# Kernel optimization log

Measured on AMD Instinct MI355X. Metric: run time of the kernel, lower is better.

Reference implementation:

```python
import jax, jax.numpy as jnp
import numpy as np
import math

B, C, H, W = 8, 64, 64, 64

def setup_inputs() -> dict:
    key = jax.random.key(0)
    k1, k2 = jax.random.split(key)
    x1 = jax.random.normal(k1, (B, C, H, W), dtype=jnp.float32)
    x2 = jax.random.normal(k2, (B, C, H, W), dtype=jnp.float32)
    return {"x1": x1, "x2": x2}

def reference(x1, x2):
    b, c, h, w = x1.shape
    # flatten spatial dims -> tokens: [B, HW, C]
    x1f = x1.reshape(b, c, h * w).transpose(0, 2, 1)
    x2f = x2.reshape(b, c, h * w).transpose(0, 2, 1)
    scale = 1.0 / math.sqrt(c)
    # direction A: queries from x1, keys/values from x2
    scores_a = jnp.einsum('bqc,bkc->bqk', x1f, x2f) * scale  # [B, HW, HW]
    out_a = jnp.einsum('bqk,bkc->bqc', jax.nn.softmax(scores_a, axis=-1), x2f)
    # direction B: queries from x2, keys/values from x1
    scores_b = jnp.einsum('bqc,bkc->bqk', x2f, x1f) * scale
    out_b = jnp.einsum('bqk,bkc->bqc', jax.nn.softmax(scores_b, axis=-1), x1f)
    out = (out_a + out_b).transpose(0, 2, 1).reshape(b, c, h, w)
    return out
```

## Files before the change

### kernel.cpp

```cpp
#include <hip/hip_runtime.h>
#include <hip/hip_bf16.h>
#include <stdint.h>


#define TT 4096
#define CC 64
#define NB 8

typedef float f32x4 __attribute__((ext_vector_type(4)));
typedef float f32x4a __attribute__((ext_vector_type(4), may_alias));
typedef short s16x8 __attribute__((ext_vector_type(8)));
typedef unsigned int u32x2a __attribute__((ext_vector_type(2), may_alias));
typedef unsigned int u32x4a __attribute__((ext_vector_type(4), may_alias));
typedef float f32a __attribute__((may_alias));

static __device__ __forceinline__ unsigned fbits(float x) { return __float_as_uint(x); }
static __device__ __forceinline__ ushort bf16of(float v) {
    return (ushort)((fbits(v) + 0x8000u) >> 16);
}
static __device__ __forceinline__ unsigned pack2(float a, float b) {
    return __builtin_amdgcn_perm(fbits(b) + 0x8000u, fbits(a) + 0x8000u, 0x07060302u);
}
static __device__ __forceinline__ s16x8 load_frag(const void* p) {
    u32x4a t = *(const u32x4a*)p;
    return __builtin_bit_cast(s16x8, t);
}

#define SQC1 0.4246609177f

__global__ void prep_k(const float* __restrict__ x1, const float* __restrict__ x2,
                       ushort* __restrict__ kt, ushort* __restrict__ vt) {
    const int inp = blockIdx.z, b = blockIdx.y, tt = blockIdx.x;
    const float* src = (inp == 0 ? x1 : x2) + (size_t)b * CC * TT;
    const size_t plane = (size_t)TT * CC;
    ushort* kd = kt + (size_t)(inp * NB + b) * plane;
    ushort* vd = vt + (size_t)(inp * NB + b) * plane;
    __shared__ ushort lds[64][72];
    const int tid = threadIdx.x;
    const int c  = tid >> 2;
    const int tg = tid & 3;
    const float* srow = src + (size_t)c * TT + tt * 64 + tg * 16;
    unsigned hw[8];
#pragma unroll
    for (int i = 0; i < 4; ++i) {
        f32x4a v = *(const f32x4a*)(srow + i * 4);
        hw[2 * i]     = pack2(v[0], v[1]);
        hw[2 * i + 1] = pack2(v[2], v[3]);
#pragma unroll
        for (int k = 0; k < 4; ++k) lds[tg * 16 + i * 4 + k][c] = bf16of(v[k] * SQC1);
    }
    {
        ushort* vchunk = vd + (((size_t)tt * 2 + (tg >> 1)) * 4 + (c >> 4)) * 512;
        const int l16v = c & 15;
        const int q0v  = (tg & 1) * 2;
        u32x4a w0 = {hw[0], hw[1], hw[2], hw[3]};
        u32x4a w1 = {hw[4], hw[5], hw[6], hw[7]};
        *(u32x4a*)(vchunk + (size_t)(q0v * 16 + l16v) * 8)       = w0;
        *(u32x4a*)(vchunk + (size_t)((q0v + 1) * 16 + l16v) * 8) = w1;
    }
    __syncthreads();
    const int mt   = tid >> 6;
    const int quad = (tid >> 4) & 3;
    const int l16  = tid & 15;
    const int t    = mt * 16 + l16;
#pragma unroll
    for (int ch = 0; ch < 2; ++ch) {
        u32x4a w = *(const u32x4a*)&lds[t][ch * 32 + quad * 8];
        *(u32x4a*)(kd + (((size_t)tt * 4 + mt) * 2 + ch) * 512 +
                   (size_t)(quad * 16 + l16) * 8) = w;
    }
}

__global__ __launch_bounds__(256, 3)
void attn_fused_k(const ushort* __restrict__ kt, const ushort* __restrict__ vt,
                  float* __restrict__ out) {
    const int b    = blockIdx.x & 7;
    const int pair = (blockIdx.x >> 3) & 1;
    const int qt   = blockIdx.x >> 4;
    const int tid  = threadIdx.x;
    const int wave = tid >> 6;
    const int lane = tid & 63;
    const int quad = lane >> 4;
    const int l16  = lane & 15;
    const int dir  = wave & 1;
    const int ks   = wave >> 1;
    const int q0   = qt * 64 + pair * 32;

    const size_t plane = (size_t)TT * CC;
    const ushort* Qp = kt + (size_t)((dir == 0 ? 0 : NB) + b) * plane + (size_t)lane * 8;
    const ushort* Kp = kt + (size_t)((dir == 0 ? NB : 0) + b) * plane + (size_t)lane * 8;
    const ushort* Vp = vt + (size_t)((dir == 0 ? NB : 0) + b) * plane + (size_t)lane * 8;

    __shared__ __align__(16) ushort pbuf[4][2][16][72];
    __shared__ float lpx[4][2][16];
    f32a* xbuf = (f32a*)&pbuf[0][0][0][0];

    s16x8 qf[2][2];
#pragma unroll
    for (int rb = 0; rb < 2; ++rb)
#pragma unroll
        for (int ch = 0; ch < 2; ++ch)
            qf[rb][ch] = load_frag(Qp + (((size_t)qt * 4 + pair * 2 + rb) * 2 + ch) * 512);

    f32x4 accO[2][4];
#pragma unroll
    for (int rb = 0; rb < 2; ++rb)
#pragma unroll
        for (int ct = 0; ct < 4; ++ct) accO[rb][ct] = (f32x4){0.f, 0.f, 0.f, 0.f};
    float lp[2] = {0.f, 0.f};

    s16x8 kA0, kA1, kA2, kA3, kA4, kA5, kA6, kA7;

    auto loadK = [&](int j) {
        const ushort* p = Kp + (size_t)(ks * 32 + j) * 4096;
        kA0 = load_frag(p);          kA1 = load_frag(p + 512);
        kA2 = load_frag(p + 1024);   kA3 = load_frag(p + 1536);
        kA4 = load_frag(p + 2048);   kA5 = load_frag(p + 2560);
        kA6 = load_frag(p + 3072);   kA7 = load_frag(p + 3584);
    };

    auto SmT = [&](s16x8 kc0, s16x8 kc1, int mt) {
#pragma unroll
        for (int rb = 0; rb < 2; ++rb) {
            f32x4 s = (f32x4){0.f, 0.f, 0.f, 0.f};
            s = __builtin_amdgcn_mfma_f32_16x16x32_bf16(kc0, qf[rb][0], s, 0, 0, 0);
            s = __builtin_amdgcn_mfma_f32_16x16x32_bf16(kc1, qf[rb][1], s, 0, 0, 0);
            float p0 = __builtin_amdgcn_exp2f(s[0]);
            float p1 = __builtin_amdgcn_exp2f(s[1]);
            float p2 = __builtin_amdgcn_exp2f(s[2]);
            float p3 = __builtin_amdgcn_exp2f(s[3]);
            lp[rb] += (p0 + p1) + (p2 + p3);
            u32x2a w;
            w[0] = pack2(p0, p1);
            w[1] = pack2(p2, p3);
            *(u32x2a*)&pbuf[wave][rb][l16][mt * 16 + quad * 4] = w;
        }
    };
    auto PVphase = [&](int j) {
        const ushort* p = Vp + (size_t)(ks * 32 + j) * 4096;
        s16x8 v0 = load_frag(p);           s16x8 v1 = load_frag(p + 512);
        s16x8 v2 = load_frag(p + 1024);    s16x8 v3 = load_frag(p + 1536);
        s16x8 v4 = load_frag(p + 2048);    s16x8 v5 = load_frag(p + 2560);
        s16x8 v6 = load_frag(p + 3072);    s16x8 v7 = load_frag(p + 3584);
        s16x8 pf0a = load_frag(&pbuf[wave][0][l16][quad * 8]);
        s16x8 pf1a = load_frag(&pbuf[wave][1][l16][quad * 8]);
        accO[0][0] = __builtin_amdgcn_mfma_f32_16x16x32_bf16(v0, pf0a, accO[0][0], 0, 0, 0);
        accO[1][0] = __builtin_amdgcn_mfma_f32_16x16x32_bf16(v0, pf1a, accO[1][0], 0, 0, 0);
        accO[0][1] = __builtin_amdgcn_mfma_f32_16x16x32_bf16(v1, pf0a, accO[0][1], 0, 0, 0);
        accO[1][1] = __builtin_amdgcn_mfma_f32_16x16x32_bf16(v1, pf1a, accO[1][1], 0, 0, 0);
        accO[0][2] = __builtin_amdgcn_mfma_f32_16x16x32_bf16(v2, pf0a, accO[0][2], 0, 0, 0);
        accO[1][2] = __builtin_amdgcn_mfma_f32_16x16x32_bf16(v2, pf1a, accO[1][2], 0, 0, 0);
        accO[0][3] = __builtin_amdgcn_mfma_f32_16x16x32_bf16(v3, pf0a, accO[0][3], 0, 0, 0);
        accO[1][3] = __builtin_amdgcn_mfma_f32_16x16x32_bf16(v3, pf1a, accO[1][3], 0, 0, 0);
        s16x8 pf0b = load_frag(&pbuf[wave][0][l16][32 + quad * 8]);
        s16x8 pf1b = load_frag(&pbuf[wave][1][l16][32 + quad * 8]);
        accO[0][0] = __builtin_amdgcn_mfma_f32_16x16x32_bf16(v4, pf0b, accO[0][0], 0, 0, 0);
        accO[1][0] = __builtin_amdgcn_mfma_f32_16x16x32_bf16(v4, pf1b, accO[1][0], 0, 0, 0);
        accO[0][1] = __builtin_amdgcn_mfma_f32_16x16x32_bf16(v5, pf0b, accO[0][1], 0, 0, 0);
        accO[1][1] = __builtin_amdgcn_mfma_f32_16x16x32_bf16(v5, pf1b, accO[1][1], 0, 0, 0);
        accO[0][2] = __builtin_amdgcn_mfma_f32_16x16x32_bf16(v6, pf0b, accO[0][2], 0, 0, 0);
        accO[1][2] = __builtin_amdgcn_mfma_f32_16x16x32_bf16(v6, pf1b, accO[1][2], 0, 0, 0);
        accO[0][3] = __builtin_amdgcn_mfma_f32_16x16x32_bf16(v7, pf0b, accO[0][3], 0, 0, 0);
        accO[1][3] = __builtin_amdgcn_mfma_f32_16x16x32_bf16(v7, pf1b, accO[1][3], 0, 0, 0);
    };

    loadK(0);
#pragma unroll 1
    for (int j = 0; j < 32; ++j) {
        __syncthreads();
        SmT(kA0, kA1, 0); SmT(kA2, kA3, 1); SmT(kA4, kA5, 2); SmT(kA6, kA7, 3);
        if (j < 31) loadK(j + 1);
        PVphase(j);
    }

    float inv[2];
#pragma unroll
    for (int rb = 0; rb < 2; ++rb) {
        float l = lp[rb];
        l += __shfl_xor(l, 16);
        l += __shfl_xor(l, 32);
        lp[rb] = l;
        if (lane < 16) lpx[wave][rb][l16] = l;
    }
    __syncthreads();
#pragma unroll
    for (int rb = 0; rb < 2; ++rb)
        inv[rb] = __builtin_amdgcn_rcpf(lp[rb] + lpx[wave ^ 2][rb][l16]);

    const int g = (ks << 1) | dir;
#pragma unroll 1
    for (int ph = 3; ph >= 1; --ph) {
        if (g == ph) {
#pragma unroll
            for (int rb = 0; rb < 2; ++rb)
#pragma unroll
                for (int ct = 0; ct < 4; ++ct)
#pragma unroll
                    for (int r = 0; r < 4; ++r) {
                        const int slot = (rb * 16 + ct * 4 + r) * 64 + lane;
                        float v = accO[rb][ct][r] * inv[rb];
                        if (ph == 3) xbuf[slot] = v;
                        else xbuf[slot] += v;
                    }
        }
        __syncthreads();
    }
    if (g == 0) {
        float* ob = out + (size_t)b * plane;
#pragma unroll
        for (int rb = 0; rb < 2; ++rb)
#pragma unroll
            for (int ct = 0; ct < 4; ++ct)
#pragma unroll
                for (int r = 0; r < 4; ++r) {
                    float v = accO[rb][ct][r] * inv[rb] +
                              xbuf[(rb * 16 + ct * 4 + r) * 64 + lane];
                    ob[(size_t)(ct * 16 + quad * 4 + r) * TT + q0 + rb * 16 + l16] = v;
                }
    }
}

extern "C" void kernel_launch(void* const* d_in, const int* in_sizes, int n_in,
                              void* d_out, int out_size, void* d_ws, size_t ws_size,
                              hipStream_t stream) {
    const float* x1 = (const float*)d_in[0];
    const float* x2 = (const float*)d_in[1];
    ushort* kt = (ushort*)d_ws;
    ushort* vt = (ushort*)d_ws + (size_t)2 * NB * TT * CC;

    hipLaunchKernelGGL(prep_k, dim3(TT / 64, NB, 2), dim3(256), 0, stream, x1, x2, kt, vt);
    hipLaunchKernelGGL(attn_fused_k, dim3(64 * NB * 2), dim3(256), 0, stream,
                       kt, vt, (float*)d_out);
}
```

Measured before the change: 180.1 us.

## Widen attention blocks to 8 waves with 64 queries and pipelined S/PV phases

```diff
diff --git a/kernel.cpp b/kernel.cpp
--- a/kernel.cpp
+++ b/kernel.cpp
@@ -71,57 +71,63 @@
     }
 }
 
-__global__ __launch_bounds__(256, 3)
+__global__ __attribute__((amdgpu_flat_work_group_size(512, 512)))
 void attn_fused_k(const ushort* __restrict__ kt, const ushort* __restrict__ vt,
                   float* __restrict__ out) {
     const int b    = blockIdx.x & 7;
-    const int pair = (blockIdx.x >> 3) & 1;
-    const int qt   = blockIdx.x >> 4;
+    const int qt   = blockIdx.x >> 3;
     const int tid  = threadIdx.x;
     const int wave = tid >> 6;
     const int lane = tid & 63;
     const int quad = lane >> 4;
     const int l16  = lane & 15;
     const int dir  = wave & 1;
-    const int ks   = wave >> 1;
-    const int q0   = qt * 64 + pair * 32;
+    const int ksq  = wave >> 1;
 
     const size_t plane = (size_t)TT * CC;
     const ushort* Qp = kt + (size_t)((dir == 0 ? 0 : NB) + b) * plane + (size_t)lane * 8;
     const ushort* Kp = kt + (size_t)((dir == 0 ? NB : 0) + b) * plane + (size_t)lane * 8;
     const ushort* Vp = vt + (size_t)((dir == 0 ? NB : 0) + b) * plane + (size_t)lane * 8;
 
-    __shared__ __align__(16) ushort pbuf[4][2][16][72];
-    __shared__ float lpx[4][2][16];
-    f32a* xbuf = (f32a*)&pbuf[0][0][0][0];
-
-    s16x8 qf[2][2];
-#pragma unroll
-    for (int rb = 0; rb < 2; ++rb)
+    __shared__ __align__(16) ushort pbuf[8][2][4][16][72];
+    __shared__ float lpx[8][4][16];
+    f32a* xbuf = (f32a*)&pbuf[0][0][0][0][0];
+
+    s16x8 qf[4][2];
+#pragma unroll
+    for (int rb = 0; rb < 4; ++rb)
 #pragma unroll
         for (int ch = 0; ch < 2; ++ch)
-            qf[rb][ch] = load_frag(Qp + (((size_t)qt * 4 + pair * 2 + rb) * 2 + ch) * 512);
-
-    f32x4 accO[2][4];
-#pragma unroll
-    for (int rb = 0; rb < 2; ++rb)
+            qf[rb][ch] = load_frag(Qp + (((size_t)qt * 4 + rb) * 2 + ch) * 512);
+
+    f32x4 accO[4][4];
+#pragma unroll
+    for (int rb = 0; rb < 4; ++rb)
 #pragma unroll
         for (int ct = 0; ct < 4; ++ct) accO[rb][ct] = (f32x4){0.f, 0.f, 0.f, 0.f};
-    float lp[2] = {0.f, 0.f};
-
-    s16x8 kA0, kA1, kA2, kA3, kA4, kA5, kA6, kA7;
+    float lp[4] = {0.f, 0.f, 0.f, 0.f};
+
+    s16x8 k0, k1, k2, k3, k4, k5, k6, k7;
+    s16x8 v0, v1, v2, v3, v4, v5, v6, v7;
 
     auto loadK = [&](int j) {
-        const ushort* p = Kp + (size_t)(ks * 32 + j) * 4096;
-        kA0 = load_frag(p);          kA1 = load_frag(p + 512);
-        kA2 = load_frag(p + 1024);   kA3 = load_frag(p + 1536);
-        kA4 = load_frag(p + 2048);   kA5 = load_frag(p + 2560);
-        kA6 = load_frag(p + 3072);   kA7 = load_frag(p + 3584);
-    };
-
-    auto SmT = [&](s16x8 kc0, s16x8 kc1, int mt) {
-#pragma unroll
-        for (int rb = 0; rb < 2; ++rb) {
+        const ushort* p = Kp + (size_t)(ksq * 16 + j) * 4096;
+        k0 = load_frag(p);          k1 = load_frag(p + 512);
+        k2 = load_frag(p + 1024);   k3 = load_frag(p + 1536);
+        k4 = load_frag(p + 2048);   k5 = load_frag(p + 2560);
+        k6 = load_frag(p + 3072);   k7 = load_frag(p + 3584);
+    };
+    auto loadV = [&](int j) {
+        const ushort* p = Vp + (size_t)(ksq * 16 + j) * 4096;
+        v0 = load_frag(p);          v1 = load_frag(p + 512);
+        v2 = load_frag(p + 1024);   v3 = load_frag(p + 1536);
+        v4 = load_frag(p + 2048);   v5 = load_frag(p + 2560);
+        v6 = load_frag(p + 3072);   v7 = load_frag(p + 3584);
+    };
+
+    auto SmT = [&](s16x8 kc0, s16x8 kc1, int mt, int par) {
+#pragma unroll
+        for (int rb = 0; rb < 4; ++rb) {
             f32x4 s = (f32x4){0.f, 0.f, 0.f, 0.f};
             s = __builtin_amdgcn_mfma_f32_16x16x32_bf16(kc0, qf[rb][0], s, 0, 0, 0);
             s = __builtin_amdgcn_mfma_f32_16x16x32_bf16(kc1, qf[rb][1], s, 0, 0, 0);
@@ -133,49 +139,54 @@
             u32x2a w;
             w[0] = pack2(p0, p1);
             w[1] = pack2(p2, p3);
-            *(u32x2a*)&pbuf[wave][rb][l16][mt * 16 + quad * 4] = w;
-        }
-    };
-    auto PVphase = [&](int j) {
-        const ushort* p = Vp + (size_t)(ks * 32 + j) * 4096;
-        s16x8 v0 = load_frag(p);           s16x8 v1 = load_frag(p + 512);
-        s16x8 v2 = load_frag(p + 1024);    s16x8 v3 = load_frag(p + 1536);
-        s16x8 v4 = load_frag(p + 2048);    s16x8 v5 = load_frag(p + 2560);
-        s16x8 v6 = load_frag(p + 3072);    s16x8 v7 = load_frag(p + 3584);
-        s16x8 pf0a = load_frag(&pbuf[wave][0][l16][quad * 8]);
-        s16x8 pf1a = load_frag(&pbuf[wave][1][l16][quad * 8]);
-        accO[0][0] = __builtin_amdgcn_mfma_f32_16x16x32_bf16(v0, pf0a, accO[0][0], 0, 0, 0);
-        accO[1][0] = __builtin_amdgcn_mfma_f32_16x16x32_bf16(v0, pf1a, accO[1][0], 0, 0, 0);
-        accO[0][1] = __builtin_amdgcn_mfma_f32_16x16x32_bf16(v1, pf0a, accO[0][1], 0, 0, 0);
-        accO[1][1] = __builtin_amdgcn_mfma_f32_16x16x32_bf16(v1, pf1a, accO[1][1], 0, 0, 0);
-        accO[0][2] = __builtin_amdgcn_mfma_f32_16x16x32_bf16(v2, pf0a, accO[0][2], 0, 0, 0);
-        accO[1][2] = __builtin_amdgcn_mfma_f32_16x16x32_bf16(v2, pf1a, accO[1][2], 0, 0, 0);
-        accO[0][3] = __builtin_amdgcn_mfma_f32_16x16x32_bf16(v3, pf0a, accO[0][3], 0, 0, 0);
-        accO[1][3] = __builtin_amdgcn_mfma_f32_16x16x32_bf16(v3, pf1a, accO[1][3], 0, 0, 0);
-        s16x8 pf0b = load_frag(&pbuf[wave][0][l16][32 + quad * 8]);
-        s16x8 pf1b = load_frag(&pbuf[wave][1][l16][32 + quad * 8]);
-        accO[0][0] = __builtin_amdgcn_mfma_f32_16x16x32_bf16(v4, pf0b, accO[0][0], 0, 0, 0);
-        accO[1][0] = __builtin_amdgcn_mfma_f32_16x16x32_bf16(v4, pf1b, accO[1][0], 0, 0, 0);
-        accO[0][1] = __builtin_amdgcn_mfma_f32_16x16x32_bf16(v5, pf0b, accO[0][1], 0, 0, 0);
-        accO[1][1] = __builtin_amdgcn_mfma_f32_16x16x32_bf16(v5, pf1b, accO[1][1], 0, 0, 0);
-        accO[0][2] = __builtin_amdgcn_mfma_f32_16x16x32_bf16(v6, pf0b, accO[0][2], 0, 0, 0);
-        accO[1][2] = __builtin_amdgcn_mfma_f32_16x16x32_bf16(v6, pf1b, accO[1][2], 0, 0, 0);
-        accO[0][3] = __builtin_amdgcn_mfma_f32_16x16x32_bf16(v7, pf0b, accO[0][3], 0, 0, 0);
-        accO[1][3] = __builtin_amdgcn_mfma_f32_16x16x32_bf16(v7, pf1b, accO[1][3], 0, 0, 0);
+            *(u32x2a*)&pbuf[wave][par][rb][l16][mt * 16 + quad * 4] = w;
+        }
+    };
+    auto Sphase = [&](int par) {
+        SmT(k0, k1, 0, par); SmT(k2, k3, 1, par);
+        SmT(k4, k5, 2, par); SmT(k6, k7, 3, par);
+    };
+
+    auto PVphase = [&](int par) {
+        s16x8 pfa[4], pfb[4];
+#pragma unroll
+        for (int rb = 0; rb < 4; ++rb)
+            pfa[rb] = load_frag(&pbuf[wave][par][rb][l16][quad * 8]);
+#pragma unroll
+        for (int rb = 0; rb < 4; ++rb) {
+            accO[rb][0] = __builtin_amdgcn_mfma_f32_16x16x32_bf16(v0, pfa[rb], accO[rb][0], 0, 0, 0);
+            accO[rb][1] = __builtin_amdgcn_mfma_f32_16x16x32_bf16(v1, pfa[rb], accO[rb][1], 0, 0, 0);
+            accO[rb][2] = __builtin_amdgcn_mfma_f32_16x16x32_bf16(v2, pfa[rb], accO[rb][2], 0, 0, 0);
+            accO[rb][3] = __builtin_amdgcn_mfma_f32_16x16x32_bf16(v3, pfa[rb], accO[rb][3], 0, 0, 0);
+        }
+#pragma unroll
+        for (int rb = 0; rb < 4; ++rb)
+            pfb[rb] = load_frag(&pbuf[wave][par][rb][l16][32 + quad * 8]);
+#pragma unroll
+        for (int rb = 0; rb < 4; ++rb) {
+            accO[rb][0] = __builtin_amdgcn_mfma_f32_16x16x32_bf16(v4, pfb[rb], accO[rb][0], 0, 0, 0);
+            accO[rb][1] = __builtin_amdgcn_mfma_f32_16x16x32_bf16(v5, pfb[rb], accO[rb][1], 0, 0, 0);
+            accO[rb][2] = __builtin_amdgcn_mfma_f32_16x16x32_bf16(v6, pfb[rb], accO[rb][2], 0, 0, 0);
+            accO[rb][3] = __builtin_amdgcn_mfma_f32_16x16x32_bf16(v7, pfb[rb], accO[rb][3], 0, 0, 0);
+        }
     };
 
     loadK(0);
 #pragma unroll 1
-    for (int j = 0; j < 32; ++j) {
-        __syncthreads();
-        SmT(kA0, kA1, 0); SmT(kA2, kA3, 1); SmT(kA4, kA5, 2); SmT(kA6, kA7, 3);
-        if (j < 31) loadK(j + 1);
-        PVphase(j);
-    }
-
-    float inv[2];
-#pragma unroll
-    for (int rb = 0; rb < 2; ++rb) {
+    for (int j = 0; j < 16; j += 2) {
+        Sphase(0);
+        loadK(j + 1);
+        if (j > 0) PVphase(1);
+        loadV(j);
+        Sphase(1);
+        if (j + 2 < 16) loadK(j + 2);
+        PVphase(0);
+        loadV(j + 1);
+    }
+    PVphase(1);
+
+#pragma unroll
+    for (int rb = 0; rb < 4; ++rb) {
         float l = lp[rb];
         l += __shfl_xor(l, 16);
         l += __shfl_xor(l, 32);
@@ -183,39 +194,42 @@
         if (lane < 16) lpx[wave][rb][l16] = l;
     }
     __syncthreads();
-#pragma unroll
-    for (int rb = 0; rb < 2; ++rb)
-        inv[rb] = __builtin_amdgcn_rcpf(lp[rb] + lpx[wave ^ 2][rb][l16]);
-
-    const int g = (ks << 1) | dir;
+    float inv[4];
+#pragma unroll
+    for (int rb = 0; rb < 4; ++rb) {
+        float l = lpx[dir][rb][l16] + lpx[2 + dir][rb][l16] +
+                  lpx[4 + dir][rb][l16] + lpx[6 + dir][rb][l16];
+        inv[rb] = __builtin_amdgcn_rcpf(l);
+    }
+
 #pragma unroll 1
-    for (int ph = 3; ph >= 1; --ph) {
-        if (g == ph) {
-#pragma unroll
-            for (int rb = 0; rb < 2; ++rb)
+    for (int ph = 7; ph >= 1; --ph) {
+        if (wave == ph) {
+#pragma unroll
+            for (int rb = 0; rb < 4; ++rb)
 #pragma unroll
                 for (int ct = 0; ct < 4; ++ct)
 #pragma unroll
                     for (int r = 0; r < 4; ++r) {
                         const int slot = (rb * 16 + ct * 4 + r) * 64 + lane;
                         float v = accO[rb][ct][r] * inv[rb];
-                        if (ph == 3) xbuf[slot] = v;
+                        if (ph == 7) xbuf[slot] = v;
                         else xbuf[slot] += v;
                     }
         }
         __syncthreads();
     }
-    if (g == 0) {
+    if (wave == 0) {
         float* ob = out + (size_t)b * plane;
 #pragma unroll
-        for (int rb = 0; rb < 2; ++rb)
+        for (int rb = 0; rb < 4; ++rb)
 #pragma unroll
             for (int ct = 0; ct < 4; ++ct)
 #pragma unroll
                 for (int r = 0; r < 4; ++r) {
                     float v = accO[rb][ct][r] * inv[rb] +
                               xbuf[(rb * 16 + ct * 4 + r) * 64 + lane];
-                    ob[(size_t)(ct * 16 + quad * 4 + r) * TT + q0 + rb * 16 + l16] = v;
+                    ob[(size_t)(ct * 16 + quad * 4 + r) * TT + qt * 64 + rb * 16 + l16] = v;
                 }
     }
 }
@@ -229,6 +243,6 @@
     ushort* vt = (ushort*)d_ws + (size_t)2 * NB * TT * CC;
 
     hipLaunchKernelGGL(prep_k, dim3(TT / 64, NB, 2), dim3(256), 0, stream, x1, x2, kt, vt);
-    hipLaunchKernelGGL(attn_fused_k, dim3(64 * NB * 2), dim3(256), 0, stream,
+    hipLaunchKernelGGL(attn_fused_k, dim3(64 * NB), dim3(512), 0, stream,
                        kt, vt, (float*)d_out);
 }
```

New measurement: 281.7 us. 56.4% more time.
